# Kernel optimization log

Measured on AMD Instinct MI355X. Metric: run time of the kernel, lower is better.

The kernel has to match this reference:

```python
import jax, jax.numpy as jnp
import numpy as np

B = 1024       # batch of graphs
NUM = 512      # predicates / nodes per graph
D = 64         # embedding_dim
H = 64         # hidden_dim
E = 4096       # edges per graph (shared structure across batch)
MAIN_NUM = 10  # softmax segment [0, MAIN_NUM); sigmoid on the rest


def setup_inputs() -> dict:
    key = jax.random.key(0)
    ks = jax.random.split(key, 8)
    x = jax.random.uniform(ks[0], (B, NUM), dtype=jnp.float32)
    embedding = jax.random.normal(ks[1], (NUM, D), dtype=jnp.float32) * 0.1
    W1 = jax.random.normal(ks[2], (D, H), dtype=jnp.float32) * (1.0 / np.sqrt(D))
    b1 = jnp.zeros((H,), jnp.float32)
    W2 = jax.random.normal(ks[3], (H, H), dtype=jnp.float32) * (1.0 / np.sqrt(H))
    b2 = jnp.zeros((H,), jnp.float32)
    W3 = jax.random.normal(ks[4], (H, 1), dtype=jnp.float32) * (1.0 / np.sqrt(H))
    b3 = jnp.zeros((1,), jnp.float32)
    edge_row = jax.random.randint(ks[5], (E,), 0, NUM, dtype=jnp.int32)
    edge_col = jax.random.randint(ks[6], (E,), 0, NUM, dtype=jnp.int32)
    return {"x": x, "embedding": embedding, "W1": W1, "b1": b1,
            "W2": W2, "b2": b2, "W3": W3, "b3": b3,
            "edge_row": edge_row, "edge_col": edge_col}


def _gcn_layer(h, W, b, row, col, norm):
    # h: [B, NUM, in]; GCNConv = linear -> D^{-1/2} A D^{-1/2} aggregate -> +bias
    hW = jnp.einsum('bni,io->bno', h, W)                 # [B, NUM, out]
    msg = hW[:, row, :] * norm[None, :, None]            # [B, E, out]
    agg = jnp.zeros_like(hW).at[:, col, :].add(msg)      # scatter to targets
    return agg + b


def reference(x, embedding, W1, b1, W2, b2, W3, b3, edge_row, edge_col):
    num = x.shape[1]
    # symmetric GCN normalization (add_self_loops=False, unit edge weights)
    deg = jnp.zeros((num,), x.dtype).at[edge_col].add(1.0)
    dinv = jnp.where(deg > 0, jax.lax.rsqrt(jnp.maximum(deg, 1.0)), 0.0)
    norm = dinv[edge_row] * dinv[edge_col]               # [E]

    h = x[..., None] * embedding                         # [B, NUM, D]
    h = jax.nn.relu(_gcn_layer(h, W1, b1, edge_row, edge_col, norm))
    h = jax.nn.relu(_gcn_layer(h, W2, b2, edge_row, edge_col, norm))
    logits = _gcn_layer(h, W3, b3, edge_row, edge_col, norm)[..., 0]  # [B, NUM]

    # convert_to_confidence: softmax over multiclass segment, sigmoid elsewhere
    phi_sm = jax.nn.softmax(logits[:, :MAIN_NUM], axis=1)
    phi_sg = jax.nn.sigmoid(logits[:, MAIN_NUM:])
    return jnp.concatenate([phi_sm, phi_sg], axis=1)
```

## Files before the change

### kernel.cpp

```cpp
#include <hip/hip_runtime.h>
#include <stdint.h>

#define NB    1024
#define NUM   512
#define HD    64
#define NE    4096
#define NEP   4608
#define MAIN  10
#define HBS   72

typedef __attribute__((ext_vector_type(8))) short short8;
typedef __attribute__((ext_vector_type(4))) float f32x4;

__device__ __forceinline__ short f2bf(float f) {
    uint32_t u = __float_as_uint(f);
    u += 0x7fffu + ((u >> 16) & 1u);
    return (short)(u >> 16);
}
__device__ __forceinline__ float bf2f(short s) {
    return __uint_as_float(((uint32_t)(uint16_t)s) << 16);
}

__global__ __launch_bounds__(512) void prep_all(
    const int* __restrict__ erow, const int* __restrict__ ecol,
    const float* __restrict__ emb, const float* __restrict__ W1,
    const float* __restrict__ W2,
    int* __restrict__ rsptr, int* __restrict__ colmap, int* __restrict__ epk,
    short* __restrict__ E1, short* __restrict__ W2T)
{
    const int t = threadIdx.x;
    if (blockIdx.x != 0) {
        int g = (blockIdx.x - 1) * 512 + t;
        if (g < NUM * HD) {
            int node = g >> 6, dim = g & 63;
            float acc = 0.0f;
            #pragma unroll
            for (int k = 0; k < HD; ++k) acc += emb[node * HD + k] * W1[k * HD + dim];
            E1[g] = f2bf(acc);
        } else if (g < NUM * HD + HD * HD) {
            int j = g - NUM * HD;
            int dout = j >> 6, din = j & 63;
            W2T[j] = f2bf(W2[din * HD + dout]);
        }
        return;
    }

    __shared__ int   sdeg[NUM];
    __shared__ int   aux[NUM];
    __shared__ float sdv[NUM];
    __shared__ int   rnk[NUM];
    __shared__ int   rdg[NUM];
    __shared__ int   wsum[8];

    const int lane = t & 63, wv = t >> 6;

    sdeg[t] = 0; aux[t] = 0;
    __syncthreads();
    for (int e = t; e < NE; e += 512) atomicAdd(&sdeg[ecol[e]], 1);
    __syncthreads();
    const int deg  = sdeg[t];
    const int pdeg = (deg + 1) & ~1;
    const int dbin = deg < NUM ? deg : NUM - 1;
    sdv[t] = deg > 0 ? rsqrtf((float)deg) : 0.0f;
    atomicAdd(&aux[dbin], 1);
    __syncthreads();
    {
        int v = aux[t];
        #pragma unroll
        for (int ofs = 1; ofs < 64; ofs <<= 1) {
            int sh = __shfl_up(v, ofs, 64);
            if (lane >= ofs) v += sh;
        }
        if (lane == 63) wsum[wv] = v;
        __syncthreads();
        if (t == 0) {
            int s = 0;
            #pragma unroll
            for (int w = 0; w < 8; ++w) { int tmp = wsum[w]; wsum[w] = s; s += tmp; }
        }
        __syncthreads();
        int inc = v + wsum[wv];
        sdeg[t] = inc - ((dbin == t) ? 0 : 0);
        aux[t]  = inc;
        __syncthreads();
        sdeg[t] = (t == 0) ? 0 : aux[t - 1];
        __syncthreads();
    }
    {
        int r = atomicAdd(&sdeg[dbin], 1);
        rnk[t] = r;
        rdg[r] = pdeg;
        colmap[r] = t;
    }
    __syncthreads();
    {
        int dv = rdg[t], v = dv;
        #pragma unroll
        for (int ofs = 1; ofs < 64; ofs <<= 1) {
            int sh = __shfl_up(v, ofs, 64);
            if (lane >= ofs) v += sh;
        }
        if (lane == 63) wsum[wv] = v;
        __syncthreads();
        if (t == 0) {
            int s = 0;
            #pragma unroll
            for (int w = 0; w < 8; ++w) { int tmp = wsum[w]; wsum[w] = s; s += tmp; }
        }
        __syncthreads();
        int inc  = v + wsum[wv];
        int excl = inc - dv;
        rsptr[t] = excl;
        if (t == NUM - 1) rsptr[NUM] = inc;
        aux[t] = excl;
        __syncthreads();
    }
    sdeg[t] = aux[rnk[t]];
    __syncthreads();
    for (int i = t; i < NEP; i += 512) epk[i] = 0;
    __syncthreads();
    for (int e = t; e < NE; e += 512) {
        int c = ecol[e], rr = erow[e];
        int p = atomicAdd(&sdeg[c], 1);
        unsigned nb = (unsigned short)f2bf(sdv[rr] * sdv[c]);
        epk[p] = (rr << 16) | (int)nb;
    }
}

__global__ __launch_bounds__(1024, 4) void gcn_body(
    const float* __restrict__ x, const short* __restrict__ E1,
    const short* __restrict__ W2T,
    const float* __restrict__ b1, const float* __restrict__ b2,
    const float* __restrict__ W3, const float* __restrict__ b3,
    const int* __restrict__ rsptrg, const int* __restrict__ colmap,
    const int* __restrict__ epkg,
    float* __restrict__ out)
{
    __shared__ short HA[NUM * HD];
    __shared__ short HB[NUM * HBS];
    __shared__ int   eps[NEP];
    __shared__ int   sptr[513];
    __shared__ float sred[2];

    float* tv   = (float*)HB;
    float* slog = ((float*)HB) + NUM;

    const int t     = threadIdx.x;
    const int b     = blockIdx.x;
    const int lane  = t & 63;
    const int wave  = t >> 6;
    const int q     = lane >> 4;
    const int l15   = lane & 15;
    const int grp   = lane >> 3;
    const int dbase = (lane & 7) * 8;

    {
        const int4* g4 = (const int4*)epkg;
        *(int4*)&eps[t * 4] = g4[t];
        if (t < 128) *(int4*)&eps[4096 + t * 4] = g4[1024 + t];
    }
    if (t < 513) sptr[t] = rsptrg[t];

    #pragma unroll
    for (int p = 0; p < 4; ++p) {
        int i = t + p * 1024;
        int r = i >> 3, d8 = (i & 7) * 8;
        float xr = x[b * NUM + r];
        short8 e = *(const short8*)&E1[r * HD + d8];
        short8 o;
        #pragma unroll
        for (int j = 0; j < 8; ++j) o[j] = f2bf(xr * bf2f(e[j]));
        *(short8*)&HA[r * HD + d8] = o;
    }

    float b1v[8], b2v[8], w3v[8];
    {
        f32x4 u0 = *(const f32x4*)&b1[dbase], u1 = *(const f32x4*)&b1[dbase + 4];
        f32x4 v0 = *(const f32x4*)&b2[dbase], v1 = *(const f32x4*)&b2[dbase + 4];
        f32x4 w0 = *(const f32x4*)&W3[dbase], w1 = *(const f32x4*)&W3[dbase + 4];
        #pragma unroll
        for (int j = 0; j < 4; ++j) {
            b1v[j] = u0[j]; b1v[j + 4] = u1[j];
            b2v[j] = v0[j]; b2v[j + 4] = v1[j];
            w3v[j] = w0[j]; w3v[j + 4] = w1[j];
        }
    }
    __syncthreads();

#define EDGE_MAC(pe)                                                          \
    {                                                                         \
        float n = __uint_as_float((unsigned)(pe) << 16);                      \
        uint4 hv = *(const uint4*)&HA[((unsigned)(pe) >> 16) * HD + dbase];   \
        a[0] = fmaf(n, __uint_as_float(hv.x << 16), a[0]);                    \
        a[1] = fmaf(n, __uint_as_float(hv.x), a[1]);                          \
        a[2] = fmaf(n, __uint_as_float(hv.y << 16), a[2]);                    \
        a[3] = fmaf(n, __uint_as_float(hv.y), a[3]);                          \
        a[4] = fmaf(n, __uint_as_float(hv.z << 16), a[4]);                    \
        a[5] = fmaf(n, __uint_as_float(hv.z), a[5]);                          \
        a[6] = fmaf(n, __uint_as_float(hv.w << 16), a[6]);                    \
        a[7] = fmaf(n, __uint_as_float(hv.w), a[7]);                          \
    }

    #pragma unroll 1
    for (int set = 0; set < 4; ++set) {
        int r  = set * 128 + wave * 8 + grp;
        int e0 = sptr[r], e1 = sptr[r + 1];
        int c  = colmap[r];
        float a[8];
        #pragma unroll
        for (int j = 0; j < 8; ++j) a[j] = 0.0f;
        int e = e0;
        for (; e + 4 <= e1; e += 4) {
            int2 pa = *(const int2*)&eps[e];
            int2 pb = *(const int2*)&eps[e + 2];
            EDGE_MAC(pa.x); EDGE_MAC(pa.y); EDGE_MAC(pb.x); EDGE_MAC(pb.y);
        }
        if (e < e1) {
            int2 pa = *(const int2*)&eps[e];
            EDGE_MAC(pa.x); EDGE_MAC(pa.y);
        }
        short8 o;
        #pragma unroll
        for (int j = 0; j < 8; ++j) o[j] = f2bf(fmaxf(a[j] + b1v[j], 0.0f));
        *(short8*)&HB[c * HBS + dbase] = o;
    }
    __syncthreads();

    {
        short8 bfr[2][4];
        #pragma unroll
        for (int ks = 0; ks < 2; ++ks)
            #pragma unroll
            for (int nt = 0; nt < 4; ++nt)
                bfr[ks][nt] = *(const short8*)&W2T[(nt * 16 + l15) * HD + ks * 32 + q * 8];
        f32x4 acc[2][4];
        #pragma unroll
        for (int mt = 0; mt < 2; ++mt)
            #pragma unroll
            for (int nt = 0; nt < 4; ++nt) acc[mt][nt] = (f32x4){0.f, 0.f, 0.f, 0.f};
        const int mbase = wave * 32;
        #pragma unroll
        for (int mt = 0; mt < 2; ++mt)
            #pragma unroll
            for (int ks = 0; ks < 2; ++ks) {
                short8 af = *(const short8*)&HB[(mbase + mt * 16 + l15) * HBS
                                                + ks * 32 + q * 8];
                #pragma unroll
                for (int nt = 0; nt < 4; ++nt)
                    acc[mt][nt] = __builtin_amdgcn_mfma_f32_16x16x32_bf16(
                        af, bfr[ks][nt], acc[mt][nt], 0, 0, 0);
            }
        #pragma unroll
        for (int mt = 0; mt < 2; ++mt)
            #pragma unroll
            for (int nt = 0; nt < 4; ++nt)
                #pragma unroll
                for (int i = 0; i < 4; ++i)
                    HA[(mbase + mt * 16 + q * 4 + i) * HD + nt * 16 + l15] =
                        f2bf(acc[mt][nt][i]);
    }
    __syncthreads();

    #pragma unroll 1
    for (int set = 0; set < 4; ++set) {
        int r  = set * 128 + wave * 8 + grp;
        int e0 = sptr[r], e1 = sptr[r + 1];
        int c  = colmap[r];
        float a[8];
        #pragma unroll
        for (int j = 0; j < 8; ++j) a[j] = 0.0f;
        int e = e0;
        for (; e + 4 <= e1; e += 4) {
            int2 pa = *(const int2*)&eps[e];
            int2 pb = *(const int2*)&eps[e + 2];
            EDGE_MAC(pa.x); EDGE_MAC(pa.y); EDGE_MAC(pb.x); EDGE_MAC(pb.y);
        }
        if (e < e1) {
            int2 pa = *(const int2*)&eps[e];
            EDGE_MAC(pa.x); EDGE_MAC(pa.y);
        }
        float v = 0.0f;
        #pragma unroll
        for (int j = 0; j < 8; ++j)
            v += fmaxf(a[j] + b2v[j], 0.0f) * w3v[j];
        v += __shfl_xor(v, 1, 64);
        v += __shfl_xor(v, 2, 64);
        v += __shfl_xor(v, 4, 64);
        if ((lane & 7) == 0) tv[c] = v;
    }
    __syncthreads();

    if (t < NUM) {
        int e0 = sptr[t], e1 = sptr[t + 1];
        float a = 0.0f;
        for (int e = e0; e < e1; ++e) {
            unsigned pe = (unsigned)eps[e];
            a = fmaf(__uint_as_float(pe << 16), tv[pe >> 16], a);
        }
        slog[colmap[t]] = a + b3[0];
    }
    __syncthreads();

    if (t < 64) {
        float v = (t < MAIN) ? slog[t] : -1e30f;
        float m = v;
        m = fmaxf(m, __shfl_xor(m, 1, 64));
        m = fmaxf(m, __shfl_xor(m, 2, 64));
        m = fmaxf(m, __shfl_xor(m, 4, 64));
        m = fmaxf(m, __shfl_xor(m, 8, 64));
        float ev = (t < MAIN) ? __expf(v - m) : 0.0f;
        ev += __shfl_xor(ev, 1, 64);
        ev += __shfl_xor(ev, 2, 64);
        ev += __shfl_xor(ev, 4, 64);
        ev += __shfl_xor(ev, 8, 64);
        if (t == 0) { sred[0] = m; sred[1] = ev; }
    }
    __syncthreads();

    if (t < NUM) {
        float l = slog[t];
        float o = (t < MAIN) ? __expf(l - sred[0]) / sred[1]
                             : 1.0f / (1.0f + __expf(-l));
        out[b * NUM + t] = o;
    }
#undef EDGE_MAC
}

extern "C" void kernel_launch(void* const* d_in, const int* in_sizes, int n_in,
                              void* d_out, int out_size, void* d_ws, size_t ws_size,
                              hipStream_t stream) {
    const float* x    = (const float*)d_in[0];
    const float* emb  = (const float*)d_in[1];
    const float* W1   = (const float*)d_in[2];
    const float* b1   = (const float*)d_in[3];
    const float* W2   = (const float*)d_in[4];
    const float* b2   = (const float*)d_in[5];
    const float* W3   = (const float*)d_in[6];
    const float* b3   = (const float*)d_in[7];
    const int*   erow = (const int*)d_in[8];
    const int*   ecol = (const int*)d_in[9];

    char* ws = (char*)d_ws;
    int*   rsptr  = (int*)ws;
    int*   colmap = (int*)(ws + 2176);
    int*   epk    = (int*)(ws + 4224);
    short* E1     = (short*)(ws + 22656);
    short* W2T    = (short*)(ws + 88192);

    prep_all<<<73, 512, 0, stream>>>(erow, ecol, emb, W1, W2,
                                     rsptr, colmap, epk, E1, W2T);
    gcn_body<<<NB, 1024, 0, stream>>>(x, E1, W2T, b1, b2, W3, b3,
                                      rsptr, colmap, epk, (float*)d_out);
}
```

Baseline: 157.4 us.

## Balance edge work across waves and fuse embedding-W1 product into main kernel via MFMA

The CSR prep kernel now computes per-wave row ranges that split the padded edge count evenly across 16 waves, replacing the fixed round-robin row assignment that left waves with unequal degree sums. The embedding×W1 precompute and the W2 transpose leave the prep kernel. The first layer's linear transform is now done per graph inside the main kernel with MFMA on x·emb, and W2 is converted to bf16 per block. The column map is also staged into LDS. This cuts the prep kernel's extra blocks and gives better load balance, at the cost of redundant per-block MFMA work and uncoalesced strided W1/W2 loads in every block.

```diff
diff --git a/kernel.cpp b/kernel.cpp
--- a/kernel.cpp
+++ b/kernel.cpp
@@ -21,37 +21,20 @@
     return __uint_as_float(((uint32_t)(uint16_t)s) << 16);
 }
 
-__global__ __launch_bounds__(512) void prep_all(
+__global__ __launch_bounds__(512) void prep_csr(
     const int* __restrict__ erow, const int* __restrict__ ecol,
-    const float* __restrict__ emb, const float* __restrict__ W1,
-    const float* __restrict__ W2,
     int* __restrict__ rsptr, int* __restrict__ colmap, int* __restrict__ epk,
-    short* __restrict__ E1, short* __restrict__ W2T)
+    int* __restrict__ wsplit)
 {
-    const int t = threadIdx.x;
-    if (blockIdx.x != 0) {
-        int g = (blockIdx.x - 1) * 512 + t;
-        if (g < NUM * HD) {
-            int node = g >> 6, dim = g & 63;
-            float acc = 0.0f;
-            #pragma unroll
-            for (int k = 0; k < HD; ++k) acc += emb[node * HD + k] * W1[k * HD + dim];
-            E1[g] = f2bf(acc);
-        } else if (g < NUM * HD + HD * HD) {
-            int j = g - NUM * HD;
-            int dout = j >> 6, din = j & 63;
-            W2T[j] = f2bf(W2[din * HD + dout]);
-        }
-        return;
-    }
-
     __shared__ int   sdeg[NUM];
     __shared__ int   aux[NUM];
+    __shared__ int   rcsr[NUM + 1];
     __shared__ float sdv[NUM];
     __shared__ int   rnk[NUM];
     __shared__ int   rdg[NUM];
     __shared__ int   wsum[8];
 
+    const int t = threadIdx.x;
     const int lane = t & 63, wv = t >> 6;
 
     sdeg[t] = 0; aux[t] = 0;
@@ -79,9 +62,7 @@
             for (int w = 0; w < 8; ++w) { int tmp = wsum[w]; wsum[w] = s; s += tmp; }
         }
         __syncthreads();
-        int inc = v + wsum[wv];
-        sdeg[t] = inc - ((dbin == t) ? 0 : 0);
-        aux[t]  = inc;
+        aux[t] = v + wsum[wv];
         __syncthreads();
         sdeg[t] = (t == 0) ? 0 : aux[t - 1];
         __syncthreads();
@@ -110,12 +91,22 @@
         __syncthreads();
         int inc  = v + wsum[wv];
         int excl = inc - dv;
+        rcsr[t] = excl;
         rsptr[t] = excl;
-        if (t == NUM - 1) rsptr[NUM] = inc;
-        aux[t] = excl;
-        __syncthreads();
-    }
-    sdeg[t] = aux[rnk[t]];
+        if (t == NUM - 1) { rcsr[NUM] = inc; rsptr[NUM] = inc; }
+        __syncthreads();
+    }
+    if (t <= 16) {
+        if (t == 0)       wsplit[0]  = 0;
+        else if (t == 16) wsplit[16] = NUM;
+        else {
+            int target = (int)(((long)t * rcsr[NUM]) / 16);
+            int r = 0;
+            while (r < NUM && rcsr[r] < target) r += 8;
+            wsplit[t] = r;
+        }
+    }
+    sdeg[t] = rcsr[rnk[t]];
     __syncthreads();
     for (int i = t; i < NEP; i += 512) epk[i] = 0;
     __syncthreads();
@@ -128,18 +119,20 @@
 }
 
 __global__ __launch_bounds__(1024, 4) void gcn_body(
-    const float* __restrict__ x, const short* __restrict__ E1,
-    const short* __restrict__ W2T,
+    const float* __restrict__ x, const float* __restrict__ emb,
+    const float* __restrict__ W1, const float* __restrict__ W2,
     const float* __restrict__ b1, const float* __restrict__ b2,
     const float* __restrict__ W3, const float* __restrict__ b3,
-    const int* __restrict__ rsptrg, const int* __restrict__ colmap,
-    const int* __restrict__ epkg,
+    const int* __restrict__ rsptrg, const int* __restrict__ colmapg,
+    const int* __restrict__ epkg, const int* __restrict__ wsplitg,
     float* __restrict__ out)
 {
     __shared__ short HA[NUM * HD];
     __shared__ short HB[NUM * HBS];
     __shared__ int   eps[NEP];
     __shared__ int   sptr[513];
+    __shared__ int   scm[NUM];
+    __shared__ int   swp[17];
     __shared__ float sred[2];
 
     float* tv   = (float*)HB;
@@ -160,17 +153,55 @@
         if (t < 128) *(int4*)&eps[4096 + t * 4] = g4[1024 + t];
     }
     if (t < 513) sptr[t] = rsptrg[t];
-
-    #pragma unroll
-    for (int p = 0; p < 4; ++p) {
-        int i = t + p * 1024;
-        int r = i >> 3, d8 = (i & 7) * 8;
-        float xr = x[b * NUM + r];
-        short8 e = *(const short8*)&E1[r * HD + d8];
-        short8 o;
-        #pragma unroll
-        for (int j = 0; j < 8; ++j) o[j] = f2bf(xr * bf2f(e[j]));
-        *(short8*)&HA[r * HD + d8] = o;
+    if (t < NUM) scm[t] = colmapg[t];
+    if (t < 17)  swp[t] = wsplitg[t];
+
+    {
+        short8 bfr[2][4];
+        #pragma unroll
+        for (int ks = 0; ks < 2; ++ks)
+            #pragma unroll
+            for (int nt = 0; nt < 4; ++nt) {
+                short8 v;
+                #pragma unroll
+                for (int j = 0; j < 8; ++j)
+                    v[j] = f2bf(W1[(ks * 32 + q * 8 + j) * HD + nt * 16 + l15]);
+                bfr[ks][nt] = v;
+            }
+        f32x4 acc[2][4];
+        #pragma unroll
+        for (int mt = 0; mt < 2; ++mt)
+            #pragma unroll
+            for (int nt = 0; nt < 4; ++nt) acc[mt][nt] = (f32x4){0.f, 0.f, 0.f, 0.f};
+        const int mbase = wave * 32;
+        #pragma unroll
+        for (int mt = 0; mt < 2; ++mt) {
+            int r = mbase + mt * 16 + l15;
+            float xr = x[b * NUM + r];
+            #pragma unroll
+            for (int ks = 0; ks < 2; ++ks) {
+                const float* ep = &emb[r * HD + ks * 32 + q * 8];
+                f32x4 e0 = *(const f32x4*)ep;
+                f32x4 e1 = *(const f32x4*)(ep + 4);
+                short8 af;
+                af[0] = f2bf(xr * e0[0]); af[1] = f2bf(xr * e0[1]);
+                af[2] = f2bf(xr * e0[2]); af[3] = f2bf(xr * e0[3]);
+                af[4] = f2bf(xr * e1[0]); af[5] = f2bf(xr * e1[1]);
+                af[6] = f2bf(xr * e1[2]); af[7] = f2bf(xr * e1[3]);
+                #pragma unroll
+                for (int nt = 0; nt < 4; ++nt)
+                    acc[mt][nt] = __builtin_amdgcn_mfma_f32_16x16x32_bf16(
+                        af, bfr[ks][nt], acc[mt][nt], 0, 0, 0);
+            }
+        }
+        #pragma unroll
+        for (int mt = 0; mt < 2; ++mt)
+            #pragma unroll
+            for (int nt = 0; nt < 4; ++nt)
+                #pragma unroll
+                for (int i = 0; i < 4; ++i)
+                    HA[(mbase + mt * 16 + q * 4 + i) * HD + nt * 16 + l15] =
+                        f2bf(acc[mt][nt][i]);
     }
 
     float b1v[8], b2v[8], w3v[8];
@@ -201,11 +232,13 @@
         a[7] = fmaf(n, __uint_as_float(hv.w), a[7]);                          \
     }
 
+    const int wbeg = swp[wave], wend = swp[wave + 1];
+
     #pragma unroll 1
-    for (int set = 0; set < 4; ++set) {
-        int r  = set * 128 + wave * 8 + grp;
+    for (int base = wbeg; base < wend; base += 8) {
+        int r  = base + grp;
         int e0 = sptr[r], e1 = sptr[r + 1];
-        int c  = colmap[r];
+        int c  = scm[r];
         float a[8];
         #pragma unroll
         for (int j = 0; j < 8; ++j) a[j] = 0.0f;
@@ -231,8 +264,13 @@
         #pragma unroll
         for (int ks = 0; ks < 2; ++ks)
             #pragma unroll
-            for (int nt = 0; nt < 4; ++nt)
-                bfr[ks][nt] = *(const short8*)&W2T[(nt * 16 + l15) * HD + ks * 32 + q * 8];
+            for (int nt = 0; nt < 4; ++nt) {
+                short8 v;
+                #pragma unroll
+                for (int j = 0; j < 8; ++j)
+                    v[j] = f2bf(W2[(ks * 32 + q * 8 + j) * HD + nt * 16 + l15]);
+                bfr[ks][nt] = v;
+            }
         f32x4 acc[2][4];
         #pragma unroll
         for (int mt = 0; mt < 2; ++mt)
@@ -262,10 +300,10 @@
     __syncthreads();
 
     #pragma unroll 1
-    for (int set = 0; set < 4; ++set) {
-        int r  = set * 128 + wave * 8 + grp;
+    for (int base = wbeg; base < wend; base += 8) {
+        int r  = base + grp;
         int e0 = sptr[r], e1 = sptr[r + 1];
-        int c  = colmap[r];
+        int c  = scm[r];
         float a[8];
         #pragma unroll
         for (int j = 0; j < 8; ++j) a[j] = 0.0f;
@@ -297,7 +335,7 @@
             unsigned pe = (unsigned)eps[e];
             a = fmaf(__uint_as_float(pe << 16), tv[pe >> 16], a);
         }
-        slog[colmap[t]] = a + b3[0];
+        slog[scm[t]] = a + b3[0];
     }
     __syncthreads();
 
@@ -341,14 +379,13 @@
     const int*   ecol = (const int*)d_in[9];
 
     char* ws = (char*)d_ws;
-    int*   rsptr  = (int*)ws;
-    int*   colmap = (int*)(ws + 2176);
-    int*   epk    = (int*)(ws + 4224);
-    short* E1     = (short*)(ws + 22656);
-    short* W2T    = (short*)(ws + 88192);
-
-    prep_all<<<73, 512, 0, stream>>>(erow, ecol, emb, W1, W2,
-                                     rsptr, colmap, epk, E1, W2T);
-    gcn_body<<<NB, 1024, 0, stream>>>(x, E1, W2T, b1, b2, W3, b3,
-                                      rsptr, colmap, epk, (float*)d_out);
-}
+    int* rsptr  = (int*)ws;
+    int* colmap = (int*)(ws + 2176);
+    int* epk    = (int*)(ws + 4224);
+    int* wsplit = (int*)(ws + 22656);
+
+    prep_csr<<<1, 512, 0, stream>>>(erow, ecol, rsptr, colmap, epk, wsplit);
+    gcn_body<<<NB, 1024, 0, stream>>>(x, emb, W1, W2, b1, b2, W3, b3,
+                                      rsptr, colmap, epk, wsplit,
+                                      (float*)d_out);
+}
```

After: 184.5 us. +17.2%, slower.

## Balance edge work across waves using precomputed degree-based row splits

Applied to the files above, without the earlier changes.

Replaces the fixed interleaved assignment of rows to waves in both aggregation passes with contiguous row ranges per wave. The ranges are chosen in the prep kernel from the prefix sum of padded degrees so that each wave gets roughly equal edge counts. This aims to remove load imbalance between waves in the gather phases. It also swaps round-to-nearest bf16 conversion for truncation via byte_perm when packing HA and HB, which is cheaper but changes rounding behaviour.

```diff
diff --git a/kernel.cpp b/kernel.cpp
--- a/kernel.cpp
+++ b/kernel.cpp
@@ -26,7 +26,7 @@
     const float* __restrict__ emb, const float* __restrict__ W1,
     const float* __restrict__ W2,
     int* __restrict__ rsptr, int* __restrict__ colmap, int* __restrict__ epk,
-    short* __restrict__ E1, short* __restrict__ W2T)
+    int* __restrict__ wsplit, short* __restrict__ E1, short* __restrict__ W2T)
 {
     const int t = threadIdx.x;
     if (blockIdx.x != 0) {
@@ -51,6 +51,7 @@
     __shared__ int   rnk[NUM];
     __shared__ int   rdg[NUM];
     __shared__ int   wsum[8];
+    __shared__ int   stot;
 
     const int lane = t & 63, wv = t >> 6;
 
@@ -79,9 +80,7 @@
             for (int w = 0; w < 8; ++w) { int tmp = wsum[w]; wsum[w] = s; s += tmp; }
         }
         __syncthreads();
-        int inc = v + wsum[wv];
-        sdeg[t] = inc - ((dbin == t) ? 0 : 0);
-        aux[t]  = inc;
+        aux[t] = v + wsum[wv];
         __syncthreads();
         sdeg[t] = (t == 0) ? 0 : aux[t - 1];
         __syncthreads();
@@ -111,9 +110,19 @@
         int inc  = v + wsum[wv];
         int excl = inc - dv;
         rsptr[t] = excl;
-        if (t == NUM - 1) rsptr[NUM] = inc;
-        aux[t] = excl;
-        __syncthreads();
+        aux[t]   = excl;
+        if (t == NUM - 1) { rsptr[NUM] = inc; stot = inc; }
+        __syncthreads();
+    }
+    if (t <= 16) {
+        if (t == 0)       wsplit[0]  = 0;
+        else if (t == 16) wsplit[16] = NUM;
+        else {
+            int target = (int)(((long)t * stot) / 16);
+            int r = 0;
+            while (r < NUM && aux[r] < target) r += 8;
+            wsplit[t] = r;
+        }
     }
     sdeg[t] = aux[rnk[t]];
     __syncthreads();
@@ -133,13 +142,14 @@
     const float* __restrict__ b1, const float* __restrict__ b2,
     const float* __restrict__ W3, const float* __restrict__ b3,
     const int* __restrict__ rsptrg, const int* __restrict__ colmap,
-    const int* __restrict__ epkg,
+    const int* __restrict__ epkg, const int* __restrict__ wsplitg,
     float* __restrict__ out)
 {
     __shared__ short HA[NUM * HD];
     __shared__ short HB[NUM * HBS];
     __shared__ int   eps[NEP];
     __shared__ int   sptr[513];
+    __shared__ int   swp[17];
     __shared__ float sred[2];
 
     float* tv   = (float*)HB;
@@ -160,6 +170,7 @@
         if (t < 128) *(int4*)&eps[4096 + t * 4] = g4[1024 + t];
     }
     if (t < 513) sptr[t] = rsptrg[t];
+    if (t < 17)  swp[t] = wsplitg[t];
 
     #pragma unroll
     for (int p = 0; p < 4; ++p) {
@@ -167,10 +178,18 @@
         int r = i >> 3, d8 = (i & 7) * 8;
         float xr = x[b * NUM + r];
         short8 e = *(const short8*)&E1[r * HD + d8];
-        short8 o;
-        #pragma unroll
-        for (int j = 0; j < 8; ++j) o[j] = f2bf(xr * bf2f(e[j]));
-        *(short8*)&HA[r * HD + d8] = o;
+        unsigned w0, w1, w2, w3;
+        {
+            float p0 = xr * bf2f(e[0]), p1 = xr * bf2f(e[1]);
+            float p2 = xr * bf2f(e[2]), p3 = xr * bf2f(e[3]);
+            float p4 = xr * bf2f(e[4]), p5 = xr * bf2f(e[5]);
+            float p6 = xr * bf2f(e[6]), p7 = xr * bf2f(e[7]);
+            w0 = __byte_perm(__float_as_uint(p0), __float_as_uint(p1), 0x7632);
+            w1 = __byte_perm(__float_as_uint(p2), __float_as_uint(p3), 0x7632);
+            w2 = __byte_perm(__float_as_uint(p4), __float_as_uint(p5), 0x7632);
+            w3 = __byte_perm(__float_as_uint(p6), __float_as_uint(p7), 0x7632);
+        }
+        *(uint4*)&HA[r * HD + d8] = make_uint4(w0, w1, w2, w3);
     }
 
     float b1v[8], b2v[8], w3v[8];
@@ -201,9 +220,11 @@
         a[7] = fmaf(n, __uint_as_float(hv.w), a[7]);                          \
     }
 
+    const int wbeg = swp[wave], wend = swp[wave + 1];
+
     #pragma unroll 1
-    for (int set = 0; set < 4; ++set) {
-        int r  = set * 128 + wave * 8 + grp;
+    for (int base = wbeg; base < wend; base += 8) {
+        int r  = base + grp;
         int e0 = sptr[r], e1 = sptr[r + 1];
         int c  = colmap[r];
         float a[8];
@@ -219,10 +240,15 @@
             int2 pa = *(const int2*)&eps[e];
             EDGE_MAC(pa.x); EDGE_MAC(pa.y);
         }
-        short8 o;
-        #pragma unroll
-        for (int j = 0; j < 8; ++j) o[j] = f2bf(fmaxf(a[j] + b1v[j], 0.0f));
-        *(short8*)&HB[c * HBS + dbase] = o;
+        float v0 = fmaxf(a[0] + b1v[0], 0.0f), v1 = fmaxf(a[1] + b1v[1], 0.0f);
+        float v2 = fmaxf(a[2] + b1v[2], 0.0f), v3 = fmaxf(a[3] + b1v[3], 0.0f);
+        float v4 = fmaxf(a[4] + b1v[4], 0.0f), v5 = fmaxf(a[5] + b1v[5], 0.0f);
+        float v6 = fmaxf(a[6] + b1v[6], 0.0f), v7 = fmaxf(a[7] + b1v[7], 0.0f);
+        unsigned w0 = __byte_perm(__float_as_uint(v0), __float_as_uint(v1), 0x7632);
+        unsigned w1 = __byte_perm(__float_as_uint(v2), __float_as_uint(v3), 0x7632);
+        unsigned w2 = __byte_perm(__float_as_uint(v4), __float_as_uint(v5), 0x7632);
+        unsigned w3 = __byte_perm(__float_as_uint(v6), __float_as_uint(v7), 0x7632);
+        *(uint4*)&HB[c * HBS + dbase] = make_uint4(w0, w1, w2, w3);
     }
     __syncthreads();
 
@@ -262,8 +288,8 @@
     __syncthreads();
 
     #pragma unroll 1
-    for (int set = 0; set < 4; ++set) {
-        int r  = set * 128 + wave * 8 + grp;
+    for (int base = wbeg; base < wend; base += 8) {
+        int r  = base + grp;
         int e0 = sptr[r], e1 = sptr[r + 1];
         int c  = colmap[r];
         float a[8];
@@ -344,11 +370,13 @@
     int*   rsptr  = (int*)ws;
     int*   colmap = (int*)(ws + 2176);
     int*   epk    = (int*)(ws + 4224);
-    short* E1     = (short*)(ws + 22656);
-    short* W2T    = (short*)(ws + 88192);
+    int*   wsplit = (int*)(ws + 22656);
+    short* E1     = (short*)(ws + 22784);
+    short* W2T    = (short*)(ws + 88320);
 
     prep_all<<<73, 512, 0, stream>>>(erow, ecol, emb, W1, W2,
-                                     rsptr, colmap, epk, E1, W2T);
+                                     rsptr, colmap, epk, wsplit, E1, W2T);
     gcn_body<<<NB, 1024, 0, stream>>>(x, E1, W2T, b1, b2, W3, b3,
-                                      rsptr, colmap, epk, (float*)d_out);
-}
+                                      rsptr, colmap, epk, wsplit,
+                                      (float*)d_out);
+}
```

After: 159.2 us. No clear change (+1.1%).
